# Kernel optimization log

Measured on AMD Instinct MI355X. Metric: run time of the kernel, lower is better.

## Reference

```python
import jax, jax.numpy as jnp
import numpy as np
import math

N_EMBED = 2048
N_HEAD = 16
HEAD_DIM = N_EMBED // N_HEAD  # 128
ROPE_BASE = 10000.0


def _rope_tables(T, dim, dtype):
    # inv_freq over even indices, emb = concat(freqs, freqs) along last dim
    inv_freq = 1.0 / (ROPE_BASE ** (jnp.arange(0, dim, 2, dtype=jnp.float32) / dim))
    t = jnp.arange(T, dtype=jnp.float32)
    freqs = jnp.einsum('i,j->ij', t, inv_freq)          # [T, dim/2]
    emb = jnp.concatenate([freqs, freqs], axis=-1)      # [T, dim]
    return jnp.cos(emb).astype(dtype), jnp.sin(emb).astype(dtype)


def _rotate_half(x):
    h = x.shape[-1] // 2
    return jnp.concatenate([-x[..., h:], x[..., :h]], axis=-1)


def setup_inputs() -> dict:
    key = jax.random.key(0)
    ks = jax.random.split(key, 5)
    B, T, C = 32, 256, N_EMBED
    s = 1.0 / math.sqrt(C)
    return {
        'x': jax.random.normal(ks[0], (B, T, C), dtype=jnp.float32),
        'wq': jax.random.normal(ks[1], (C, C), dtype=jnp.float32) * s,
        'wk': jax.random.normal(ks[2], (C, C), dtype=jnp.float32) * s,
        'wv': jax.random.normal(ks[3], (C, C), dtype=jnp.float32) * s,
        'wo': jax.random.normal(ks[4], (C, C), dtype=jnp.float32) * s,
    }


def reference(x, wq, wk, wv, wo):
    B, T, C = x.shape
    H, D = N_HEAD, HEAD_DIM
    # torch Linear: y = x @ W^T
    q = (x @ wq.T).reshape(B, T, H, D).transpose(0, 2, 1, 3)  # [B,H,T,D]
    k = (x @ wk.T).reshape(B, T, H, D).transpose(0, 2, 1, 3)
    v = (x @ wv.T).reshape(B, T, H, D).transpose(0, 2, 1, 3)

    cos, sin = _rope_tables(T, D, x.dtype)  # [T,D] each, broadcast over B,H
    q = q * cos + _rotate_half(q) * sin
    k = k * cos + _rotate_half(k) * sin

    att = jnp.einsum('bhqd,bhkd->bhqk', q, k) / math.sqrt(D)
    causal = jnp.triu(jnp.ones((T, T), dtype=bool), k=1)
    att = jnp.where(causal, jnp.finfo(att.dtype).min, att)
    att = jax.nn.softmax(att, axis=-1)
    # dropout p=0.0 -> identity
    y = jnp.einsum('bhqk,bhkd->bhqd', att, v)
    y = y.transpose(0, 2, 1, 3).reshape(B, T, C)
    return y @ wo.T
```

## Files before the change

kernel.cpp:

```cpp
#include <hip/hip_runtime.h>

#define HB 32
#define HT 256
#define HC 2048
#define HH 16
#define HD 128
#define HM (HB * HT)

typedef __bf16 bf16x8 __attribute__((ext_vector_type(8)));
typedef float f32x4 __attribute__((ext_vector_type(4)));

__device__ __forceinline__ unsigned short f2bf(float f) {
  unsigned u = __float_as_uint(f);
  u += 0x7FFFu + ((u >> 16) & 1u);
  return (unsigned short)(u >> 16);
}

__global__ __launch_bounds__(256) void cvt_all(
    const float* __restrict__ x, const float* __restrict__ wq, const float* __restrict__ wk,
    const float* __restrict__ wv, const float* __restrict__ wo,
    unsigned short* __restrict__ xb, unsigned short* __restrict__ wqb,
    unsigned short* __restrict__ wkb, unsigned short* __restrict__ wvb,
    unsigned short* __restrict__ wob) {
  size_t i = (size_t)blockIdx.x * 256 + threadIdx.x;
  const float* src;
  unsigned short* dst;
  size_t off;
  if (i < 4194304) {
    src = x; dst = xb; off = i;
  } else {
    size_t j = i - 4194304;
    int w = (int)(j >> 20);
    off = j & 1048575;
    src = (w == 0) ? wq : (w == 1) ? wk : (w == 2) ? wv : wo;
    dst = (w == 0) ? wqb : (w == 1) ? wkb : (w == 2) ? wvb : wob;
  }
  float4 v = ((const float4*)src)[off];
  ushort4 o;
  o.x = f2bf(v.x); o.y = f2bf(v.y); o.z = f2bf(v.z); o.w = f2bf(v.w);
  ((ushort4*)dst)[off] = o;
}

__device__ __forceinline__ void gl_lds16(const unsigned short* g, unsigned short* l) {
  __builtin_amdgcn_global_load_lds((const __attribute__((address_space(1))) void*)g,
                                   (__attribute__((address_space(3))) void*)l, 16, 0, 0);
}

__device__ __forceinline__ int nfcol(int wn, int nf) {
  return (wn >> 1) * 128 + (wn & 1) * 32 + (nf & 1) * 16 + (nf >> 1) * 64;
}

__device__ __forceinline__ void stage_tile(const unsigned short* __restrict__ A,
                                           const unsigned short* __restrict__ W,
                                           unsigned short* dA, unsigned short* dW,
                                           int kt, int tid) {
#pragma unroll
  for (int i = 0; i < 2; i++) {
    int c = i * 512 + tid;
    int row = c >> 2, slot = c & 3;
    int gc = slot ^ ((row >> 1) & 3);
    gl_lds16(A + (size_t)row * HC + kt * 32 + gc * 8, dA + c * 8);
  }
#pragma unroll
  for (int i = 0; i < 2; i++) {
    int c = i * 512 + tid;
    int row = c >> 2, slot = c & 3;
    int gc = slot ^ ((row >> 1) & 3);
    gl_lds16(W + (size_t)row * HC + kt * 32 + gc * 8, dW + c * 8);
  }
}

#define NTILES 64

__device__ __forceinline__ void gemm_core8(const unsigned short* __restrict__ A,
                                           const unsigned short* __restrict__ W,
                                           unsigned short* lsA, unsigned short* lsB,
                                           f32x4 acc[8][4], int tid) {
  const int lane = tid & 63;
  const int l16 = lane & 15, quad = lane >> 4;
  const int wave = tid >> 6;
  const int wm = wave >> 2, wn = wave & 3;

  stage_tile(A, W, lsA, lsB, 0, tid);
  stage_tile(A, W, lsA + 8192, lsB + 8192, 1, tid);
  stage_tile(A, W, lsA + 16384, lsB + 16384, 2, tid);
  asm volatile("s_waitcnt vmcnt(8)");
  __builtin_amdgcn_s_barrier();

  for (int t = 0; t < NTILES; ++t) {
    const int cur = t & 3;
    const unsigned short* cA = lsA + cur * 8192;
    const unsigned short* cB = lsB + cur * 8192;
    if (t + 3 < NTILES) {
      const int nb = (t + 3) & 3;
      stage_tile(A, W, lsA + nb * 8192, lsB + nb * 8192, t + 3, tid);
    }
    bf16x8 af[8], bfr[4];
#pragma unroll
    for (int mf = 0; mf < 8; mf++) {
      int row = wm * 128 + mf * 16 + l16;
      int slot = quad ^ ((row >> 1) & 3);
      af[mf] = *(const bf16x8*)(cA + row * 32 + slot * 8);
    }
#pragma unroll
    for (int nf = 0; nf < 4; nf++) {
      int row = nfcol(wn, nf) + l16;
      int slot = quad ^ ((row >> 1) & 3);
      bfr[nf] = *(const bf16x8*)(cB + row * 32 + slot * 8);
    }
    __builtin_amdgcn_s_setprio(1);
#pragma unroll
    for (int mf = 0; mf < 8; mf++)
#pragma unroll
      for (int nf = 0; nf < 4; nf++)
        acc[mf][nf] = __builtin_amdgcn_mfma_f32_16x16x32_bf16(af[mf], bfr[nf], acc[mf][nf], 0, 0, 0);
    __builtin_amdgcn_s_setprio(0);
    if (t < NTILES - 3) {
      asm volatile("s_waitcnt vmcnt(8)");
    } else if (t == NTILES - 3) {
      asm volatile("s_waitcnt vmcnt(4)");
    } else if (t == NTILES - 2) {
      asm volatile("s_waitcnt vmcnt(0)");
    }
    __builtin_amdgcn_s_barrier();
  }
}

__global__ __launch_bounds__(512, 2) void gemm_out(const unsigned short* __restrict__ A,
                                                   const unsigned short* __restrict__ W,
                                                   float* __restrict__ outp) {
  __shared__ __align__(16) unsigned short lsA[32768];
  __shared__ __align__(16) unsigned short lsB[32768];
  const int tid = threadIdx.x;
  const int lane = tid & 63, wave = tid >> 6;
  const int l16 = lane & 15, quad = lane >> 4;
  const int wm = wave >> 2, wn = wave & 3;
  const int bm = blockIdx.x, bn = blockIdx.y;

  f32x4 acc[8][4];
#pragma unroll
  for (int i = 0; i < 8; i++)
#pragma unroll
    for (int j = 0; j < 4; j++) acc[i][j] = f32x4{0.f, 0.f, 0.f, 0.f};

  gemm_core8(A + (size_t)bm * 256 * HC, W + (size_t)bn * 256 * HC, lsA, lsB, acc, tid);

#pragma unroll
  for (int mf = 0; mf < 8; mf++)
#pragma unroll
    for (int nf = 0; nf < 4; nf++) {
      const int n = bn * 256 + nfcol(wn, nf) + l16;
#pragma unroll
      for (int r = 0; r < 4; r++) {
        const int m = bm * 256 + wm * 128 + mf * 16 + quad * 4 + r;
        outp[(size_t)m * HC + n] = acc[mf][nf][r];
      }
    }
}

__global__ __launch_bounds__(512, 2) void gemm_qkv(const unsigned short* __restrict__ A,
                                                   const unsigned short* __restrict__ W0,
                                                   const unsigned short* __restrict__ W1,
                                                   const unsigned short* __restrict__ W2,
                                                   unsigned short* __restrict__ Qo,
                                                   unsigned short* __restrict__ Ko,
                                                   unsigned short* __restrict__ Vto) {
  __shared__ __align__(16) unsigned short lsA[32768];
  __shared__ __align__(16) unsigned short lsB[32768];
  const int tid = threadIdx.x;
  const int lane = tid & 63, wave = tid >> 6;
  const int l16 = lane & 15, quad = lane >> 4;
  const int wm = wave >> 2, wn = wave & 3;
  const int bm = blockIdx.x;
  const int which = blockIdx.y >> 3;
  const int bn = blockIdx.y & 7;

  f32x4 acc[8][4];
#pragma unroll
  for (int i = 0; i < 8; i++)
#pragma unroll
    for (int j = 0; j < 4; j++) acc[i][j] = f32x4{0.f, 0.f, 0.f, 0.f};

  if (which < 2) {
    const unsigned short* W = (which == 0) ? W0 : W1;
    unsigned short* outp = (which == 0) ? Qo : Ko;
    gemm_core8(A + (size_t)bm * 256 * HC, W + (size_t)bn * 256 * HC, lsA, lsB, acc, tid);
    const int h = bn * 2 + (wn >> 1);
#pragma unroll
    for (int p = 0; p < 2; p++) {
      const int d = (wn & 1) * 32 + p * 16 + l16;
      const float invf = __expf((float)d * (-0.14391156831212787f));
#pragma unroll
      for (int mf = 0; mf < 8; mf++)
#pragma unroll
        for (int r = 0; r < 4; r++) {
          const int m = bm * 256 + wm * 128 + mf * 16 + quad * 4 + r;
          const int t = m & 255, b = m >> 8;
          float ang = (float)t * invf;
          float sn, cs;
          __sincosf(ang, &sn, &cs);
          float lo = acc[mf][p][r], hi = acc[mf][p + 2][r];
          size_t base = (((size_t)b * HH + h) * HT + t) * HD;
          outp[base + d] = f2bf(lo * cs - hi * sn);
          outp[base + 64 + d] = f2bf(hi * cs + lo * sn);
        }
    }
  } else {
    const int tok = bm;
    const int ch = bn;
    gemm_core8(W2 + (size_t)ch * 256 * HC, A + (size_t)tok * 256 * HC, lsA, lsB, acc, tid);
#pragma unroll
    for (int mf = 0; mf < 8; mf++)
#pragma unroll
      for (int nf = 0; nf < 4; nf++) {
        const int tcol = nfcol(wn, nf) + l16;
#pragma unroll
        for (int r = 0; r < 4; r++) {
          const int cabs = ch * 256 + wm * 128 + mf * 16 + quad * 4 + r;
          const int hh = cabs >> 7, d = cabs & 127;
          Vto[(((size_t)tok * HH + hh) * HD + d) * HT + tcol] = f2bf(acc[mf][nf][r]);
        }
      }
  }
}

__global__ __launch_bounds__(256) void attn_kernel(const unsigned short* __restrict__ Q,
                                                   const unsigned short* __restrict__ K,
                                                   const unsigned short* __restrict__ Vt,
                                                   unsigned short* __restrict__ Y) {
  const int g = blockIdx.x;
  const int wq = 3 - (g >> 9);
  const int bh = g & 511;
  const int wave = threadIdx.x >> 6;
  const int lane = threadIdx.x & 63;
  const int quad = lane >> 4, l16 = lane & 15;

  const unsigned short* Qh = Q + (size_t)bh * HT * HD;
  const unsigned short* Kh = K + (size_t)bh * HT * HD;
  const unsigned short* Vh = Vt + (size_t)bh * HD * HT;

  __shared__ __align__(16) unsigned short P[4][16 * 72];
  unsigned short* Pw = P[wave];

  const int qrow = wq * 64 + wave * 16;

  bf16x8 qf[4];
#pragma unroll
  for (int ks = 0; ks < 4; ks++)
    qf[ks] = *(const bf16x8*)(Qh + (size_t)(qrow + l16) * HD + ks * 32 + quad * 8);

  f32x4 o[8];
#pragma unroll
  for (int di = 0; di < 8; di++) o[di] = f32x4{0.f, 0.f, 0.f, 0.f};
  float mrow[4], lrow[4];
#pragma unroll
  for (int r = 0; r < 4; r++) { mrow[r] = -1e30f; lrow[r] = 0.f; }

  const float scale = 0.088388347648318447f;

  for (int ct = 0; ct <= wq; ++ct) {
    f32x4 s[4];
#pragma unroll
    for (int ni = 0; ni < 4; ni++) s[ni] = f32x4{0.f, 0.f, 0.f, 0.f};
    const int nimax = (ct == wq) ? wave : 3;
#pragma unroll
    for (int ks = 0; ks < 4; ks++) {
#pragma unroll
      for (int ni = 0; ni < 4; ni++) {
        if (ni <= nimax) {
          bf16x8 kf = *(const bf16x8*)(Kh + (size_t)(ct * 64 + ni * 16 + l16) * HD + ks * 32 + quad * 8);
          s[ni] = __builtin_amdgcn_mfma_f32_16x16x32_bf16(qf[ks], kf, s[ni], 0, 0, 0);
        }
      }
    }
    if (ct == wq) {
#pragma unroll
      for (int ni = 0; ni < 4; ni++)
#pragma unroll
        for (int r = 0; r < 4; r++) {
          int qr = wave * 16 + quad * 4 + r;
          int kc = ni * 16 + l16;
          s[ni][r] = (kc <= qr) ? s[ni][r] * scale : -1e30f;
        }
    } else {
#pragma unroll
      for (int ni = 0; ni < 4; ni++)
#pragma unroll
        for (int r = 0; r < 4; r++) s[ni][r] *= scale;
    }
#pragma unroll
    for (int r = 0; r < 4; r++) {
      float v = fmaxf(fmaxf(s[0][r], s[1][r]), fmaxf(s[2][r], s[3][r]));
      v = fmaxf(v, __shfl_xor(v, 1, 64));
      v = fmaxf(v, __shfl_xor(v, 2, 64));
      v = fmaxf(v, __shfl_xor(v, 4, 64));
      v = fmaxf(v, __shfl_xor(v, 8, 64));
      float mnew = fmaxf(mrow[r], v);
      float alpha = __expf(mrow[r] - mnew);
      mrow[r] = mnew;
      float rs = 0.f;
#pragma unroll
      for (int ni = 0; ni < 4; ni++) {
        float e = __expf(s[ni][r] - mnew);
        s[ni][r] = e;
        rs += e;
      }
      rs += __shfl_xor(rs, 1, 64);
      rs += __shfl_xor(rs, 2, 64);
      rs += __shfl_xor(rs, 4, 64);
      rs += __shfl_xor(rs, 8, 64);
      lrow[r] = lrow[r] * alpha + rs;
#pragma unroll
      for (int di = 0; di < 8; di++) o[di][r] *= alpha;
    }
#pragma unroll
    for (int ni = 0; ni < 4; ni++)
#pragma unroll
      for (int r = 0; r < 4; r++)
        Pw[(quad * 4 + r) * 72 + ni * 16 + l16] = f2bf(s[ni][r]);
#pragma unroll
    for (int ks = 0; ks < 2; ks++) {
      bf16x8 pf = *(const bf16x8*)(Pw + (size_t)l16 * 72 + ks * 32 + quad * 8);
#pragma unroll
      for (int di = 0; di < 8; di++) {
        bf16x8 vf = *(const bf16x8*)(Vh + (size_t)(di * 16 + l16) * HT + ct * 64 + ks * 32 + quad * 8);
        o[di] = __builtin_amdgcn_mfma_f32_16x16x32_bf16(pf, vf, o[di], 0, 0, 0);
      }
    }
  }

  const int b = bh >> 4, h = bh & 15;
#pragma unroll
  for (int r = 0; r < 4; r++) {
    float inv = 1.f / lrow[r];
    int t = qrow + quad * 4 + r;
    size_t rowb = ((size_t)b * HT + t) * HC + h * HD;
#pragma unroll
    for (int di = 0; di < 8; di++)
      Y[rowb + di * 16 + l16] = f2bf(o[di][r] * inv);
  }
}

extern "C" void kernel_launch(void* const* d_in, const int* in_sizes, int n_in,
                              void* d_out, int out_size, void* d_ws, size_t ws_size,
                              hipStream_t stream) {
  const float* x  = (const float*)d_in[0];
  const float* wq = (const float*)d_in[1];
  const float* wk = (const float*)d_in[2];
  const float* wv = (const float*)d_in[3];
  const float* wo = (const float*)d_in[4];
  float* out = (float*)d_out;

  char* ws = (char*)d_ws;
  const size_t MB = (size_t)1 << 20;
  unsigned short* wqb = (unsigned short*)(ws + 0 * MB);
  unsigned short* wkb = (unsigned short*)(ws + 8 * MB);
  unsigned short* wvb = (unsigned short*)(ws + 16 * MB);
  unsigned short* wob = (unsigned short*)(ws + 24 * MB);
  unsigned short* xb  = (unsigned short*)(ws + 32 * MB);
  unsigned short* Qb  = (unsigned short*)(ws + 64 * MB);
  unsigned short* Kb  = (unsigned short*)(ws + 96 * MB);
  unsigned short* Vtb = (unsigned short*)(ws + 128 * MB);
  unsigned short* Yb  = xb;

  cvt_all<<<32768, 256, 0, stream>>>(x, wq, wk, wv, wo, xb, wqb, wkb, wvb, wob);

  gemm_qkv<<<dim3(HM / 256, 24), 512, 0, stream>>>(xb, wqb, wkb, wvb, Qb, Kb, Vtb);

  attn_kernel<<<2048, 256, 0, stream>>>(Qb, Kb, Vtb, Yb);

  gemm_out<<<dim3(HM / 256, HC / 256), 512, 0, stream>>>(Yb, wob, out);
}
```

Measured before the change: 573.4 us.

## Split GEMM k-tile into two phases interleaving LDS reads, prefetch and MFMA

The GEMM main loop now splits each 32-wide k-tile into two phases of four M-fragments each. Each phase loads its fragments from LDS, issues half of the next global-to-LDS prefetch (A in the first phase, W in the second), then runs 16 MFMAs between barriers, in a ping-pong style schedule. The LDS swizzle changes from XOR on (row>>1)&3 to XOR on row&3, which changes the bank-conflict pattern. Each tile now takes four barriers instead of one, and the new vmcnt accounting has to stay correct across the split prefetch.

Result: faster. 545.9 us (-4.8%).

```diff
diff --git a/kernel.cpp b/kernel.cpp
--- a/kernel.cpp
+++ b/kernel.cpp
@@ -50,79 +50,77 @@
   return (wn >> 1) * 128 + (wn & 1) * 32 + (nf & 1) * 16 + (nf >> 1) * 64;
 }
 
-__device__ __forceinline__ void stage_tile(const unsigned short* __restrict__ A,
-                                           const unsigned short* __restrict__ W,
-                                           unsigned short* dA, unsigned short* dW,
-                                           int kt, int tid) {
+__device__ __forceinline__ void stage32(const unsigned short* __restrict__ src,
+                                        unsigned short* dst, int tid) {
 #pragma unroll
   for (int i = 0; i < 2; i++) {
     int c = i * 512 + tid;
     int row = c >> 2, slot = c & 3;
-    int gc = slot ^ ((row >> 1) & 3);
-    gl_lds16(A + (size_t)row * HC + kt * 32 + gc * 8, dA + c * 8);
-  }
-#pragma unroll
-  for (int i = 0; i < 2; i++) {
-    int c = i * 512 + tid;
-    int row = c >> 2, slot = c & 3;
-    int gc = slot ^ ((row >> 1) & 3);
-    gl_lds16(W + (size_t)row * HC + kt * 32 + gc * 8, dW + c * 8);
-  }
-}
-
-#define NTILES 64
+    int gc = slot ^ (row & 3);
+    gl_lds16(src + (size_t)row * HC + gc * 8, dst + c * 8);
+  }
+}
+
+#define KT 64
 
 __device__ __forceinline__ void gemm_core8(const unsigned short* __restrict__ A,
                                            const unsigned short* __restrict__ W,
                                            unsigned short* lsA, unsigned short* lsB,
                                            f32x4 acc[8][4], int tid) {
-  const int lane = tid & 63;
-  const int l16 = lane & 15, quad = lane >> 4;
-  const int wave = tid >> 6;
-  const int wm = wave >> 2, wn = wave & 3;
-
-  stage_tile(A, W, lsA, lsB, 0, tid);
-  stage_tile(A, W, lsA + 8192, lsB + 8192, 1, tid);
-  stage_tile(A, W, lsA + 16384, lsB + 16384, 2, tid);
+  const int lane = tid & 63, l16 = lane & 15, quad = lane >> 4;
+  const int wave = tid >> 6, wm = wave >> 2, wn = wave & 3;
+
+  stage32(A, lsA, tid);
+  stage32(W, lsB, tid);
+  stage32(A + 32, lsA + 8192, tid);
+  stage32(W + 32, lsB + 8192, tid);
+  stage32(A + 64, lsA + 16384, tid);
+  stage32(W + 64, lsB + 16384, tid);
   asm volatile("s_waitcnt vmcnt(8)");
   __builtin_amdgcn_s_barrier();
 
-  for (int t = 0; t < NTILES; ++t) {
-    const int cur = t & 3;
-    const unsigned short* cA = lsA + cur * 8192;
-    const unsigned short* cB = lsB + cur * 8192;
-    if (t + 3 < NTILES) {
-      const int nb = (t + 3) & 3;
-      stage_tile(A, W, lsA + nb * 8192, lsB + nb * 8192, t + 3, tid);
-    }
-    bf16x8 af[8], bfr[4];
-#pragma unroll
-    for (int mf = 0; mf < 8; mf++) {
-      int row = wm * 128 + mf * 16 + l16;
-      int slot = quad ^ ((row >> 1) & 3);
-      af[mf] = *(const bf16x8*)(cA + row * 32 + slot * 8);
-    }
-#pragma unroll
-    for (int nf = 0; nf < 4; nf++) {
-      int row = nfcol(wn, nf) + l16;
-      int slot = quad ^ ((row >> 1) & 3);
-      bfr[nf] = *(const bf16x8*)(cB + row * 32 + slot * 8);
-    }
-    __builtin_amdgcn_s_setprio(1);
-#pragma unroll
-    for (int mf = 0; mf < 8; mf++)
-#pragma unroll
-      for (int nf = 0; nf < 4; nf++)
-        acc[mf][nf] = __builtin_amdgcn_mfma_f32_16x16x32_bf16(af[mf], bfr[nf], acc[mf][nf], 0, 0, 0);
-    __builtin_amdgcn_s_setprio(0);
-    if (t < NTILES - 3) {
-      asm volatile("s_waitcnt vmcnt(8)");
-    } else if (t == NTILES - 3) {
-      asm volatile("s_waitcnt vmcnt(4)");
-    } else if (t == NTILES - 2) {
-      asm volatile("s_waitcnt vmcnt(0)");
-    }
-    __builtin_amdgcn_s_barrier();
+  for (int t = 0; t < KT; ++t) {
+    const unsigned short* cA = lsA + (t & 3) * 8192;
+    const unsigned short* cB = lsB + (t & 3) * 8192;
+    unsigned short* nA = lsA + ((t + 3) & 3) * 8192;
+    unsigned short* nB = lsB + ((t + 3) & 3) * 8192;
+    const bool pf = (t + 3 < KT);
+#pragma unroll
+    for (int ph = 0; ph < 2; ++ph) {
+      bf16x8 af[4], bfv[4];
+#pragma unroll
+      for (int mf = 0; mf < 4; ++mf) {
+        int row = wm * 128 + ph * 64 + mf * 16 + l16;
+        int ch = quad ^ (row & 3);
+        af[mf] = *(const bf16x8*)(cA + row * 32 + ch * 8);
+      }
+#pragma unroll
+      for (int nf = 0; nf < 4; ++nf) {
+        int row = nfcol(wn, nf) + l16;
+        int ch = quad ^ (row & 3);
+        bfv[nf] = *(const bf16x8*)(cB + row * 32 + ch * 8);
+      }
+      if (pf) {
+        if (ph == 0) stage32(A + (size_t)(t + 3) * 32, nA, tid);
+        else         stage32(W + (size_t)(t + 3) * 32, nB, tid);
+      }
+      if (ph == 1) {
+        const int rem = KT - 2 - t;
+        if (rem >= 2)      asm volatile("s_waitcnt vmcnt(8)");
+        else if (rem == 1) asm volatile("s_waitcnt vmcnt(4)");
+        else if (rem == 0) asm volatile("s_waitcnt vmcnt(0)");
+      }
+      __builtin_amdgcn_s_barrier();
+      __builtin_amdgcn_s_setprio(1);
+#pragma unroll
+      for (int mf = 0; mf < 4; ++mf)
+#pragma unroll
+        for (int nf = 0; nf < 4; ++nf)
+          acc[ph * 4 + mf][nf] =
+              __builtin_amdgcn_mfma_f32_16x16x32_bf16(af[mf], bfv[nf], acc[ph * 4 + mf][nf], 0, 0, 0);
+      __builtin_amdgcn_s_setprio(0);
+      __builtin_amdgcn_s_barrier();
+    }
   }
 }
 
```
